# Kernel tuning notes

Measured on AMD Instinct MI355X. Metric: run time of the kernel, lower is better.

Reference implementation:

```python
import jax, jax.numpy as jnp
import numpy as np

EMBED_DIM = 128
NUM_HEADS = 4
HEAD_DIM = EMBED_DIM // NUM_HEADS


def setup_inputs() -> dict:
    key = jax.random.key(0)
    ks = jax.random.split(key, 12)
    B, N, D = 4, 4096, EMBED_DIM
    s = 1.0 / np.sqrt(D)
    inp = {
        "query": jax.random.normal(ks[0], (B, N, D), dtype=jnp.float32),
        "key": jax.random.normal(ks[1], (B, N, D), dtype=jnp.float32),
        "value": jax.random.normal(ks[2], (B, N, D), dtype=jnp.float32),
        "Wq": jax.random.uniform(ks[3], (D, D), jnp.float32, -s, s),
        "bq": jax.random.uniform(ks[4], (D,), jnp.float32, -s, s),
        "Wk": jax.random.uniform(ks[5], (D, D), jnp.float32, -s, s),
        "bk": jax.random.uniform(ks[6], (D,), jnp.float32, -s, s),
        "Wv": jax.random.uniform(ks[7], (D, D), jnp.float32, -s, s),
        "bv": jax.random.uniform(ks[8], (D,), jnp.float32, -s, s),
        "Wo": jax.random.uniform(ks[9], (D, D), jnp.float32, -s, s),
        "bo": jax.random.uniform(ks[10], (D,), jnp.float32, -s, s),
    }
    return inp


def reference(query, key, value, Wq, bq, Wk, bk, Wv, bv, Wo, bo):
    B, N, D = query.shape
    H, Dh = NUM_HEADS, HEAD_DIM
    scale = Dh ** -0.5
    # Linear projections (torch Linear: x @ W.T + b), split heads -> [B, H, N, Dh]
    Q = (query @ Wq.T + bq).reshape(B, N, H, Dh).transpose(0, 2, 1, 3)
    K = (key @ Wk.T + bk).reshape(B, N, H, Dh).transpose(0, 2, 1, 3)
    V = (value @ Wv.T + bv).reshape(B, N, H, Dh).transpose(0, 2, 1, 3)
    # Attention scores [B, H, N, N]
    scores = jnp.einsum('bhqd,bhkd->bhqk', Q, K) * scale
    attn = jax.nn.softmax(scores, axis=-1)
    ctx = jnp.einsum('bhqk,bhkd->bhqd', attn, V)  # [B, H, N, Dh]
    ctx = ctx.transpose(0, 2, 1, 3).reshape(B, N, D)
    return ctx @ Wo.T + bo
```

## Files before the change

kernel.cpp:

```cpp
#include <hip/hip_runtime.h>
#include <hip/hip_bf16.h>

#define N_SEQ 4096
#define DIM   128
#define NH    4
#define DH    32
#define BATCH 4

#define QSCALE 0.25503495870989204f

typedef __bf16 bf16x8 __attribute__((ext_vector_type(8)));
typedef __bf16 bf16x2 __attribute__((ext_vector_type(2)));
typedef __bf16 bf16x4 __attribute__((ext_vector_type(4)));
typedef float  f32x4  __attribute__((ext_vector_type(4)));

#define MFMA(a, b, c) __builtin_amdgcn_mfma_f32_16x16x32_bf16((a), (b), (c), 0, 0, 0)

static __device__ __forceinline__ bf16x8 cvt8(const float* __restrict__ p) {
    const float4* f4 = reinterpret_cast<const float4*>(p);
    float4 a = f4[0], b = f4[1];
    bf16x8 r;
    r[0] = (__bf16)a.x; r[1] = (__bf16)a.y; r[2] = (__bf16)a.z; r[3] = (__bf16)a.w;
    r[4] = (__bf16)b.x; r[5] = (__bf16)b.y; r[6] = (__bf16)b.z; r[7] = (__bf16)b.w;
    return r;
}

static __device__ __forceinline__ f32x4 exp4(f32x4 s) {
    f32x4 r;
    r[0] = __builtin_amdgcn_exp2f(s[0]);
    r[1] = __builtin_amdgcn_exp2f(s[1]);
    r[2] = __builtin_amdgcn_exp2f(s[2]);
    r[3] = __builtin_amdgcn_exp2f(s[3]);
    return r;
}

static __device__ __forceinline__ bf16x8 pack8(f32x4 a, f32x4 b) {
    bf16x8 o;
    o[0] = (__bf16)a[0]; o[1] = (__bf16)a[1];
    o[2] = (__bf16)a[2]; o[3] = (__bf16)a[3];
    o[4] = (__bf16)b[0]; o[5] = (__bf16)b[1];
    o[6] = (__bf16)b[2]; o[7] = (__bf16)b[3];
    return o;
}

__global__ __launch_bounds__(256) void proj_qkv(
    const float* __restrict__ xq, const float* __restrict__ xk, const float* __restrict__ xv,
    const float* __restrict__ Wq, const float* __restrict__ Wk, const float* __restrict__ Wv,
    const float* __restrict__ bq, const float* __restrict__ bk, const float* __restrict__ bv,
    __bf16* __restrict__ Qs, __bf16* __restrict__ Kb, __bf16* __restrict__ Vt)
{
    __shared__ __align__(16) char wlds[34816];
    const int z = blockIdx.z;
    const float* x    = (z == 0) ? xq : ((z == 1) ? xk : xv);
    const float* Wf   = (z == 0) ? Wq : ((z == 1) ? Wk : Wv);
    const float* bias = (z == 0) ? bq : ((z == 1) ? bk : bv);
    const int b    = blockIdx.y;
    const int tid  = threadIdx.x;
    const int wave = tid >> 6, lane = tid & 63;
    const int quad = lane >> 4, l15 = lane & 15;
    const int n0   = blockIdx.x * 64 + wave * 16;

    {
        const int r = tid >> 1, half = tid & 1;
        const float* wsrc = Wf + r * DIM + half * 64;
        char* wdst = wlds + r * 272 + half * 128;
        #pragma unroll
        for (int i = 0; i < 8; i++)
            *(bf16x8*)(wdst + i * 16) = cvt8(wsrc + i * 8);
    }

    bf16x8 a[4];
    const float* xrow = x + (b * N_SEQ + n0 + l15) * DIM + quad * 8;
    a[0] = cvt8(xrow);      a[1] = cvt8(xrow + 32);
    a[2] = cvt8(xrow + 64); a[3] = cvt8(xrow + 96);
    __syncthreads();

    const int n = n0 + l15;
    for (int t = 0; t < 8; t++) {
        const char* wr = wlds + (t * 16 + l15) * 272 + quad * 16;
        bf16x8 w0 = *(const bf16x8*)(wr);
        bf16x8 w1 = *(const bf16x8*)(wr + 64);
        bf16x8 w2 = *(const bf16x8*)(wr + 128);
        bf16x8 w3 = *(const bf16x8*)(wr + 192);

        f32x4 acc = {0.f, 0.f, 0.f, 0.f};
        acc = MFMA(w0, a[0], acc);
        acc = MFMA(w1, a[1], acc);
        acc = MFMA(w2, a[2], acc);
        acc = MFMA(w3, a[3], acc);

        const int d0 = t * 16 + quad * 4;
        if (z == 0) {
            const int h = d0 >> 5, dh0 = d0 & 31;
            bf16x4 q4;
            #pragma unroll
            for (int r = 0; r < 4; r++)
                q4[r] = (__bf16)((acc[r] + bias[d0 + r]) * QSCALE);
            *(bf16x4*)(Qs + ((b * NH + h) * N_SEQ + n) * DH + dh0) = q4;
        } else if (z == 1) {
            const int h = d0 >> 5, dh0 = d0 & 31;
            bf16x4 k4;
            #pragma unroll
            for (int r = 0; r < 4; r++)
                k4[r] = (__bf16)(acc[r] + bias[d0 + r]);
            *(bf16x4*)(Kb + ((b * NH + h) * N_SEQ + n) * DH + dh0) = k4;
        } else {
            const int nl = n & 63;
            const int np = (n & ~63) | (nl & 35) | ((nl & 12) << 1) | ((nl & 16) >> 2);
            #pragma unroll
            for (int r = 0; r < 4; r++) {
                const int d = d0 + r, h = d >> 5, dh = d & 31;
                Vt[((b * NH + h) * DH + dh) * N_SEQ + np] = (__bf16)(acc[r] + bias[d]);
            }
        }
    }
}

__global__ __launch_bounds__(256, 2) void flash_attn(
    const __bf16* __restrict__ Qs, const __bf16* __restrict__ Kb,
    const __bf16* __restrict__ Vt, __bf16* __restrict__ ctxb)
{
    __shared__ __align__(16) char smem[77824];
    char* const Kbase = smem;
    char* const Vbase = smem + 40960;

    const int bid  = blockIdx.x;
    const int bh   = bid & 15;
    const int qc   = bid >> 4;
    const int tid  = threadIdx.x;
    const int wave = tid >> 6, lane = tid & 63;
    const int quad = lane >> 4, l15 = lane & 15;
    const int qh   = wave & 1, kh = wave >> 1;
    const int n0   = qc * 128 + qh * 64;
    const int KH   = 2048;

    const __bf16* Qp = Qs + (bh * N_SEQ + n0) * DH;
    bf16x8 qf[4];
    #pragma unroll
    for (int q = 0; q < 4; q++)
        qf[q] = *(const bf16x8*)(Qp + (q * 16 + l15) * DH + quad * 8);

    const int r_ = tid >> 2, c_ = tid & 3;
    const __bf16* gK = Kb + (size_t)bh * N_SEQ * DH + r_ * DH + c_ * 8;
    const __bf16* gV = Vt + ((size_t)bh * DH + (tid >> 3)) * N_SEQ + (tid & 7) * 8;
    const int kofsK = r_ * 80 + c_ * 16;
    const int kofsV = (tid >> 3) * 144 + (tid & 7) * 16;

    {
        #pragma unroll
        for (int g = 0; g < 2; g++) {
            #pragma unroll
            for (int t = 0; t < 2; t++) {
                bf16x8 kr = *(const bf16x8*)(gK + (size_t)(g * KH + t * 64) * DH);
                bf16x8 vr = *(const bf16x8*)(gV + g * KH + t * 64);
                *(bf16x8*)(Kbase + g * 20480 + t * 5120 + kofsK) = kr;
                *(bf16x8*)(Vbase + g * 18432 + t * 4608 + kofsV) = vr;
            }
        }
    }
    __syncthreads();

    char* const Kme = Kbase + kh * 20480;
    char* const Vme = Vbase + kh * 18432;

    f32x4 c[4][2];
    #pragma unroll
    for (int q = 0; q < 4; q++) { c[q][0] = f32x4{0.f,0.f,0.f,0.f}; c[q][1] = f32x4{0.f,0.f,0.f,0.f}; }
    float l[4] = {0.f, 0.f, 0.f, 0.f};
    const f32x4 z4 = {0.f,0.f,0.f,0.f};

    for (int kbb = 0; kbb < KH / 128; kbb++) {
        const int cur = kbb & 1;
        const char* Kc = Kme + cur * 10240;
        const char* Vc = Vme + cur * 9216;

        const int kn = (kbb + 1) & (KH / 128 - 1);
        bf16x8 krn[2][2], vrn[2][2];
        #pragma unroll
        for (int g = 0; g < 2; g++) {
            #pragma unroll
            for (int t = 0; t < 2; t++) {
                krn[g][t] = *(const bf16x8*)(gK + (size_t)(g * KH + kn * 128 + t * 64) * DH);
                vrn[g][t] = *(const bf16x8*)(gV + g * KH + kn * 128 + t * 64);
            }
        }

        #pragma unroll
        for (int t = 0; t < 2; t++) {
            const char* Kt  = Kc + t * 5120;
            const char* Vtl = Vc + t * 4608;

            bf16x8 kf0 = *(const bf16x8*)(Kt + l15 * 80 + quad * 16);
            bf16x8 kf1 = *(const bf16x8*)(Kt + (16 + l15) * 80 + quad * 16);
            bf16x8 kf2 = *(const bf16x8*)(Kt + (32 + l15) * 80 + quad * 16);
            bf16x8 kf3 = *(const bf16x8*)(Kt + (48 + l15) * 80 + quad * 16);

            bf16x8 pf[4][2];
            #pragma unroll
            for (int q = 0; q < 4; q++) {
                f32x4 sa = MFMA(kf0, qf[q], z4);
                f32x4 sb = MFMA(kf1, qf[q], z4);
                f32x4 sc = MFMA(kf2, qf[q], z4);
                f32x4 sd = MFMA(kf3, qf[q], z4);
                f32x4 ea = exp4(sa), eb = exp4(sb), ec = exp4(sc), ed = exp4(sd);
                l[q] += ((ea[0]+ea[1])+(ea[2]+ea[3])) + ((eb[0]+eb[1])+(eb[2]+eb[3]))
                      + ((ec[0]+ec[1])+(ec[2]+ec[3])) + ((ed[0]+ed[1])+(ed[2]+ed[3]));
                pf[q][0] = pack8(ea, eb);
                pf[q][1] = pack8(ec, ed);
            }

            bf16x8 vf00 = *(const bf16x8*)(Vtl + l15 * 144 + quad * 16);
            bf16x8 vf10 = *(const bf16x8*)(Vtl + (16 + l15) * 144 + quad * 16);
            bf16x8 vf01 = *(const bf16x8*)(Vtl + l15 * 144 + 64 + quad * 16);
            bf16x8 vf11 = *(const bf16x8*)(Vtl + (16 + l15) * 144 + 64 + quad * 16);

            #pragma unroll
            for (int q = 0; q < 4; q++) {
                c[q][0] = MFMA(vf00, pf[q][0], c[q][0]);
                c[q][1] = MFMA(vf10, pf[q][0], c[q][1]);
                c[q][0] = MFMA(vf01, pf[q][1], c[q][0]);
                c[q][1] = MFMA(vf11, pf[q][1], c[q][1]);
            }
        }

        #pragma unroll
        for (int g = 0; g < 2; g++) {
            #pragma unroll
            for (int t = 0; t < 2; t++) {
                *(bf16x8*)(Kbase + g * 20480 + (cur ^ 1) * 10240 + t * 5120 + kofsK) = krn[g][t];
                *(bf16x8*)(Vbase + g * 18432 + (cur ^ 1) * 9216 + t * 4608 + kofsV) = vrn[g][t];
            }
        }
        __syncthreads();
    }

    #pragma unroll
    for (int q = 0; q < 4; q++) {
        l[q] += __shfl_xor(l[q], 16);
        l[q] += __shfl_xor(l[q], 32);
    }

    if (kh == 1) {
        char* dst = smem + (qh * 64 + lane) * 144;
        #pragma unroll
        for (int q = 0; q < 4; q++) {
            *(f32x4*)(dst + (q * 2 + 0) * 16) = c[q][0];
            *(f32x4*)(dst + (q * 2 + 1) * 16) = c[q][1];
        }
        f32x4 lv = {l[0], l[1], l[2], l[3]};
        *(f32x4*)(dst + 128) = lv;
    }
    __syncthreads();
    if (kh == 0) {
        const char* src = smem + (qh * 64 + lane) * 144;
        f32x4 lp = *(const f32x4*)(src + 128);
        const int b = bh >> 2, h = bh & 3;
        #pragma unroll
        for (int q = 0; q < 4; q++) {
            c[q][0] += *(const f32x4*)(src + (q * 2 + 0) * 16);
            c[q][1] += *(const f32x4*)(src + (q * 2 + 1) * 16);
            const float inv = 1.0f / (l[q] + lp[q]);
            const int qg = n0 + q * 16 + l15;
            __bf16* dst = ctxb + ((size_t)(b * N_SEQ + qg)) * DIM + h * DH + quad * 4;
            #pragma unroll
            for (int dt = 0; dt < 2; dt++) {
                f32x4 cc = c[q][dt];
                bf16x2 e0 = {(__bf16)(cc[0] * inv), (__bf16)(cc[1] * inv)};
                bf16x2 e1 = {(__bf16)(cc[2] * inv), (__bf16)(cc[3] * inv)};
                *(bf16x2*)(dst + dt * 16)     = e0;
                *(bf16x2*)(dst + dt * 16 + 2) = e1;
            }
        }
    }
}

__global__ __launch_bounds__(256) void out_proj(
    const __bf16* __restrict__ ctxb, const float* __restrict__ Wo,
    const float* __restrict__ bo, float* __restrict__ out)
{
    __shared__ __align__(16) char wlds[34816];
    const int b    = blockIdx.y;
    const int tid  = threadIdx.x;
    const int wave = tid >> 6, lane = tid & 63;
    const int quad = lane >> 4, l15 = lane & 15;
    const int n0   = blockIdx.x * 64 + wave * 16;

    {
        const int r = tid >> 1, half = tid & 1;
        const float* wsrc = Wo + r * DIM + half * 64;
        char* wdst = wlds + r * 272 + half * 128;
        #pragma unroll
        for (int i = 0; i < 8; i++)
            *(bf16x8*)(wdst + i * 16) = cvt8(wsrc + i * 8);
    }

    bf16x8 a[4];
    const __bf16* crow = ctxb + (b * N_SEQ + n0 + l15) * DIM + quad * 8;
    a[0] = *(const bf16x8*)(crow);
    a[1] = *(const bf16x8*)(crow + 32);
    a[2] = *(const bf16x8*)(crow + 64);
    a[3] = *(const bf16x8*)(crow + 96);
    __syncthreads();

    const int n = n0 + l15;
    for (int t = 0; t < 8; t++) {
        const char* wr = wlds + (t * 16 + l15) * 272 + quad * 16;
        bf16x8 w0 = *(const bf16x8*)(wr);
        bf16x8 w1 = *(const bf16x8*)(wr + 64);
        bf16x8 w2 = *(const bf16x8*)(wr + 128);
        bf16x8 w3 = *(const bf16x8*)(wr + 192);

        f32x4 acc = {0.f, 0.f, 0.f, 0.f};
        acc = MFMA(w0, a[0], acc);
        acc = MFMA(w1, a[1], acc);
        acc = MFMA(w2, a[2], acc);
        acc = MFMA(w3, a[3], acc);

        const int d0 = t * 16 + quad * 4;
        float4 o;
        o.x = acc[0] + bo[d0];
        o.y = acc[1] + bo[d0 + 1];
        o.z = acc[2] + bo[d0 + 2];
        o.w = acc[3] + bo[d0 + 3];
        *(float4*)(out + (b * N_SEQ + n) * DIM + d0) = o;
    }
}

extern "C" void kernel_launch(void* const* d_in, const int* in_sizes, int n_in,
                              void* d_out, int out_size, void* d_ws, size_t ws_size,
                              hipStream_t stream)
{
    const float* query = (const float*)d_in[0];
    const float* key   = (const float*)d_in[1];
    const float* value = (const float*)d_in[2];
    const float* Wq = (const float*)d_in[3];
    const float* bq = (const float*)d_in[4];
    const float* Wk = (const float*)d_in[5];
    const float* bk = (const float*)d_in[6];
    const float* Wv = (const float*)d_in[7];
    const float* bv = (const float*)d_in[8];
    const float* Wo = (const float*)d_in[9];
    const float* bo = (const float*)d_in[10];
    float* out = (float*)d_out;

    char* ws = (char*)d_ws;
    const size_t e = (size_t)BATCH * N_SEQ * DIM;
    __bf16* Qs   = (__bf16*)(ws);
    __bf16* Kb   = (__bf16*)(ws + 2 * e);
    __bf16* Vt   = (__bf16*)(ws + 4 * e);
    __bf16* ctxb = (__bf16*)(ws + 6 * e);

    proj_qkv<<<dim3(64, BATCH, 3), 256, 0, stream>>>(
        query, key, value, Wq, Wk, Wv, bq, bk, bv, Qs, Kb, Vt);
    flash_attn<<<dim3(512), 256, 0, stream>>>(Qs, Kb, Vt, ctxb);
    out_proj<<<dim3(64, BATCH), 256, 0, stream>>>(ctxb, Wo, bo, out);
}
```

Measured before the change: 150.2 us.

## Split flash attention work across eight waves per block with 32-row query slices

Doubles the attention block to 512 threads so each wave handles 32 query rows instead of 64, halving per-wave accumulators and Q fragments. Loading is also split so the first 256 threads stage K tiles and the rest stage V tiles, giving one prefetch stream per thread. This is meant to raise waves per CU and hide MFMA/exp latency. The cost is that each K/V tile read from LDS is reused by fewer query rows, so LDS traffic per unit of work goes up, and the 76 KB of LDS per block limits how many blocks fit on a CU.

```diff
diff --git a/kernel.cpp b/kernel.cpp
--- a/kernel.cpp
+++ b/kernel.cpp
@@ -116,7 +116,7 @@
     }
 }
 
-__global__ __launch_bounds__(256, 2) void flash_attn(
+__global__ __launch_bounds__(512, 4) void flash_attn(
     const __bf16* __restrict__ Qs, const __bf16* __restrict__ Kb,
     const __bf16* __restrict__ Vt, __bf16* __restrict__ ctxb)
 {
@@ -130,31 +130,38 @@
     const int tid  = threadIdx.x;
     const int wave = tid >> 6, lane = tid & 63;
     const int quad = lane >> 4, l15 = lane & 15;
-    const int qh   = wave & 1, kh = wave >> 1;
-    const int n0   = qc * 128 + qh * 64;
+    const int qh   = wave & 3, kh = wave >> 2;
+    const int n0   = qc * 128 + qh * 32;
     const int KH   = 2048;
 
     const __bf16* Qp = Qs + (bh * N_SEQ + n0) * DH;
-    bf16x8 qf[4];
-    #pragma unroll
-    for (int q = 0; q < 4; q++)
-        qf[q] = *(const bf16x8*)(Qp + (q * 16 + l15) * DH + quad * 8);
-
-    const int r_ = tid >> 2, c_ = tid & 3;
-    const __bf16* gK = Kb + (size_t)bh * N_SEQ * DH + r_ * DH + c_ * 8;
-    const __bf16* gV = Vt + ((size_t)bh * DH + (tid >> 3)) * N_SEQ + (tid & 7) * 8;
-    const int kofsK = r_ * 80 + c_ * 16;
-    const int kofsV = (tid >> 3) * 144 + (tid & 7) * 16;
+    bf16x8 qf[2];
+    qf[0] = *(const bf16x8*)(Qp + l15 * DH + quad * 8);
+    qf[1] = *(const bf16x8*)(Qp + (16 + l15) * DH + quad * 8);
+
+    const int s = tid & 255;
+    const bool isK = (tid < 256);
+    const __bf16* gsrc;
+    char* ldsb;
+    int kofs, gstr, bstr, tstr;
+    size_t gmul;
+    if (isK) {
+        gsrc = Kb + (size_t)bh * N_SEQ * DH + (s >> 2) * DH + (s & 3) * 8;
+        ldsb = Kbase; kofs = (s >> 2) * 80 + (s & 3) * 16;
+        gstr = 20480; bstr = 10240; tstr = 5120; gmul = DH;
+    } else {
+        gsrc = Vt + ((size_t)bh * DH + (s >> 3)) * N_SEQ + (s & 7) * 8;
+        ldsb = Vbase; kofs = (s >> 3) * 144 + (s & 7) * 16;
+        gstr = 18432; bstr = 9216; tstr = 4608; gmul = 1;
+    }
 
     {
         #pragma unroll
         for (int g = 0; g < 2; g++) {
             #pragma unroll
             for (int t = 0; t < 2; t++) {
-                bf16x8 kr = *(const bf16x8*)(gK + (size_t)(g * KH + t * 64) * DH);
-                bf16x8 vr = *(const bf16x8*)(gV + g * KH + t * 64);
-                *(bf16x8*)(Kbase + g * 20480 + t * 5120 + kofsK) = kr;
-                *(bf16x8*)(Vbase + g * 18432 + t * 4608 + kofsV) = vr;
+                bf16x8 r = *(const bf16x8*)(gsrc + (size_t)(g * KH + t * 64) * gmul);
+                *(bf16x8*)(ldsb + g * gstr + t * tstr + kofs) = r;
             }
         }
     }
@@ -163,11 +170,10 @@
     char* const Kme = Kbase + kh * 20480;
     char* const Vme = Vbase + kh * 18432;
 
-    f32x4 c[4][2];
-    #pragma unroll
-    for (int q = 0; q < 4; q++) { c[q][0] = f32x4{0.f,0.f,0.f,0.f}; c[q][1] = f32x4{0.f,0.f,0.f,0.f}; }
-    float l[4] = {0.f, 0.f, 0.f, 0.f};
-    const f32x4 z4 = {0.f,0.f,0.f,0.f};
+    f32x4 c[2][2];
+    const f32x4 z4 = {0.f, 0.f, 0.f, 0.f};
+    c[0][0] = z4; c[0][1] = z4; c[1][0] = z4; c[1][1] = z4;
+    float l[2] = {0.f, 0.f};
 
     for (int kbb = 0; kbb < KH / 128; kbb++) {
         const int cur = kbb & 1;
@@ -175,14 +181,12 @@
         const char* Vc = Vme + cur * 9216;
 
         const int kn = (kbb + 1) & (KH / 128 - 1);
-        bf16x8 krn[2][2], vrn[2][2];
+        bf16x8 pre[2][2];
         #pragma unroll
         for (int g = 0; g < 2; g++) {
             #pragma unroll
-            for (int t = 0; t < 2; t++) {
-                krn[g][t] = *(const bf16x8*)(gK + (size_t)(g * KH + kn * 128 + t * 64) * DH);
-                vrn[g][t] = *(const bf16x8*)(gV + g * KH + kn * 128 + t * 64);
-            }
+            for (int t = 0; t < 2; t++)
+                pre[g][t] = *(const bf16x8*)(gsrc + (size_t)(g * KH + kn * 128 + t * 64) * gmul);
         }
 
         #pragma unroll
@@ -195,9 +199,9 @@
             bf16x8 kf2 = *(const bf16x8*)(Kt + (32 + l15) * 80 + quad * 16);
             bf16x8 kf3 = *(const bf16x8*)(Kt + (48 + l15) * 80 + quad * 16);
 
-            bf16x8 pf[4][2];
-            #pragma unroll
-            for (int q = 0; q < 4; q++) {
+            bf16x8 pf[2][2];
+            #pragma unroll
+            for (int q = 0; q < 2; q++) {
                 f32x4 sa = MFMA(kf0, qf[q], z4);
                 f32x4 sb = MFMA(kf1, qf[q], z4);
                 f32x4 sc = MFMA(kf2, qf[q], z4);
@@ -215,7 +219,7 @@
             bf16x8 vf11 = *(const bf16x8*)(Vtl + (16 + l15) * 144 + 64 + quad * 16);
 
             #pragma unroll
-            for (int q = 0; q < 4; q++) {
+            for (int q = 0; q < 2; q++) {
                 c[q][0] = MFMA(vf00, pf[q][0], c[q][0]);
                 c[q][1] = MFMA(vf10, pf[q][0], c[q][1]);
                 c[q][0] = MFMA(vf01, pf[q][1], c[q][0]);
@@ -226,40 +230,39 @@
         #pragma unroll
         for (int g = 0; g < 2; g++) {
             #pragma unroll
-            for (int t = 0; t < 2; t++) {
-                *(bf16x8*)(Kbase + g * 20480 + (cur ^ 1) * 10240 + t * 5120 + kofsK) = krn[g][t];
-                *(bf16x8*)(Vbase + g * 18432 + (cur ^ 1) * 9216 + t * 4608 + kofsV) = vrn[g][t];
-            }
+            for (int t = 0; t < 2; t++)
+                *(bf16x8*)(ldsb + g * gstr + (cur ^ 1) * bstr + t * tstr + kofs) = pre[g][t];
         }
         __syncthreads();
     }
 
     #pragma unroll
-    for (int q = 0; q < 4; q++) {
+    for (int q = 0; q < 2; q++) {
         l[q] += __shfl_xor(l[q], 16);
         l[q] += __shfl_xor(l[q], 32);
     }
 
     if (kh == 1) {
-        char* dst = smem + (qh * 64 + lane) * 144;
-        #pragma unroll
-        for (int q = 0; q < 4; q++) {
-            *(f32x4*)(dst + (q * 2 + 0) * 16) = c[q][0];
-            *(f32x4*)(dst + (q * 2 + 1) * 16) = c[q][1];
-        }
-        f32x4 lv = {l[0], l[1], l[2], l[3]};
-        *(f32x4*)(dst + 128) = lv;
+        char* dst = smem + (qh * 64 + lane) * 80;
+        #pragma unroll
+        for (int q = 0; q < 2; q++) {
+            *(f32x4*)(dst + q * 32)      = c[q][0];
+            *(f32x4*)(dst + q * 32 + 16) = c[q][1];
+        }
+        float2 lv = {l[0], l[1]};
+        *(float2*)(dst + 64) = lv;
     }
     __syncthreads();
     if (kh == 0) {
-        const char* src = smem + (qh * 64 + lane) * 144;
-        f32x4 lp = *(const f32x4*)(src + 128);
+        const char* src = smem + (qh * 64 + lane) * 80;
+        float2 lp = *(const float2*)(src + 64);
+        const float lpa[2] = {lp.x, lp.y};
         const int b = bh >> 2, h = bh & 3;
         #pragma unroll
-        for (int q = 0; q < 4; q++) {
-            c[q][0] += *(const f32x4*)(src + (q * 2 + 0) * 16);
-            c[q][1] += *(const f32x4*)(src + (q * 2 + 1) * 16);
-            const float inv = 1.0f / (l[q] + lp[q]);
+        for (int q = 0; q < 2; q++) {
+            c[q][0] += *(const f32x4*)(src + q * 32);
+            c[q][1] += *(const f32x4*)(src + q * 32 + 16);
+            const float inv = 1.0f / (l[q] + lpa[q]);
             const int qg = n0 + q * 16 + l15;
             __bf16* dst = ctxb + ((size_t)(b * N_SEQ + qg)) * DIM + h * DH + quad * 4;
             #pragma unroll
@@ -352,6 +355,6 @@
 
     proj_qkv<<<dim3(64, BATCH, 3), 256, 0, stream>>>(
         query, key, value, Wq, Wk, Wv, bq, bk, bv, Qs, Kb, Vt);
-    flash_attn<<<dim3(512), 256, 0, stream>>>(Qs, Kb, Vt, ctxb);
+    flash_attn<<<dim3(512), 512, 0, stream>>>(Qs, Kb, Vt, ctxb);
     out_proj<<<dim3(64, BATCH), 256, 0, stream>>>(ctxb, Wo, bo, out);
 }
```

New measurement: 158.2 us. +5.3%, slower.

## Compute softmax row sums with ones-matrix MFMA and prioritize MFMA issue

Applied to the files above, without the earlier changes.

Moves the softmax denominator accumulation off the VALU by multiplying the packed bf16 probabilities with a ones vector through extra MFMAs. This drops the per-element adds and the final cross-lane shuffles. All K/V LDS fragments for both sub-tiles are now loaded before compute, and MFMA sections are wrapped in s_setprio to favour matrix issue. The change adds 25% more PV-stage MFMAs, raises register pressure from the preloaded fragments, and sums the bf16-rounded probabilities rather than the fp32 ones.

```diff
diff --git a/kernel.cpp b/kernel.cpp
--- a/kernel.cpp
+++ b/kernel.cpp
@@ -140,6 +140,10 @@
     for (int q = 0; q < 4; q++)
         qf[q] = *(const bf16x8*)(Qp + (q * 16 + l15) * DH + quad * 8);
 
+    bf16x8 ones;
+    #pragma unroll
+    for (int i = 0; i < 8; i++) ones[i] = (__bf16)1.0f;
+
     const int r_ = tid >> 2, c_ = tid & 3;
     const __bf16* gK = Kb + (size_t)bh * N_SEQ * DH + r_ * DH + c_ * 8;
     const __bf16* gV = Vt + ((size_t)bh * DH + (tid >> 3)) * N_SEQ + (tid & 7) * 8;
@@ -164,10 +168,10 @@
     char* const Vme = Vbase + kh * 18432;
 
     f32x4 c[4][2];
+    f32x4 cl[4];
+    const f32x4 z4 = {0.f,0.f,0.f,0.f};
     #pragma unroll
-    for (int q = 0; q < 4; q++) { c[q][0] = f32x4{0.f,0.f,0.f,0.f}; c[q][1] = f32x4{0.f,0.f,0.f,0.f}; }
-    float l[4] = {0.f, 0.f, 0.f, 0.f};
-    const f32x4 z4 = {0.f,0.f,0.f,0.f};
+    for (int q = 0; q < 4; q++) { c[q][0] = z4; c[q][1] = z4; cl[q] = z4; }
 
     for (int kbb = 0; kbb < KH / 128; kbb++) {
         const int cur = kbb & 1;
@@ -185,42 +189,47 @@
             }
         }
 
+        bf16x8 kfa[2][4], vfa[2][4];
         #pragma unroll
         for (int t = 0; t < 2; t++) {
             const char* Kt  = Kc + t * 5120;
             const char* Vtl = Vc + t * 4608;
-
-            bf16x8 kf0 = *(const bf16x8*)(Kt + l15 * 80 + quad * 16);
-            bf16x8 kf1 = *(const bf16x8*)(Kt + (16 + l15) * 80 + quad * 16);
-            bf16x8 kf2 = *(const bf16x8*)(Kt + (32 + l15) * 80 + quad * 16);
-            bf16x8 kf3 = *(const bf16x8*)(Kt + (48 + l15) * 80 + quad * 16);
-
+            #pragma unroll
+            for (int i = 0; i < 4; i++)
+                kfa[t][i] = *(const bf16x8*)(Kt + (i * 16 + l15) * 80 + quad * 16);
+            vfa[t][0] = *(const bf16x8*)(Vtl + l15 * 144 + quad * 16);
+            vfa[t][1] = *(const bf16x8*)(Vtl + (16 + l15) * 144 + quad * 16);
+            vfa[t][2] = *(const bf16x8*)(Vtl + l15 * 144 + 64 + quad * 16);
+            vfa[t][3] = *(const bf16x8*)(Vtl + (16 + l15) * 144 + 64 + quad * 16);
+        }
+
+        #pragma unroll
+        for (int t = 0; t < 2; t++) {
             bf16x8 pf[4][2];
             #pragma unroll
             for (int q = 0; q < 4; q++) {
-                f32x4 sa = MFMA(kf0, qf[q], z4);
-                f32x4 sb = MFMA(kf1, qf[q], z4);
-                f32x4 sc = MFMA(kf2, qf[q], z4);
-                f32x4 sd = MFMA(kf3, qf[q], z4);
+                __builtin_amdgcn_s_setprio(1);
+                f32x4 sa = MFMA(kfa[t][0], qf[q], z4);
+                f32x4 sb = MFMA(kfa[t][1], qf[q], z4);
+                f32x4 sc = MFMA(kfa[t][2], qf[q], z4);
+                f32x4 sd = MFMA(kfa[t][3], qf[q], z4);
+                __builtin_amdgcn_s_setprio(0);
                 f32x4 ea = exp4(sa), eb = exp4(sb), ec = exp4(sc), ed = exp4(sd);
-                l[q] += ((ea[0]+ea[1])+(ea[2]+ea[3])) + ((eb[0]+eb[1])+(eb[2]+eb[3]))
-                      + ((ec[0]+ec[1])+(ec[2]+ec[3])) + ((ed[0]+ed[1])+(ed[2]+ed[3]));
                 pf[q][0] = pack8(ea, eb);
                 pf[q][1] = pack8(ec, ed);
             }
 
-            bf16x8 vf00 = *(const bf16x8*)(Vtl + l15 * 144 + quad * 16);
-            bf16x8 vf10 = *(const bf16x8*)(Vtl + (16 + l15) * 144 + quad * 16);
-            bf16x8 vf01 = *(const bf16x8*)(Vtl + l15 * 144 + 64 + quad * 16);
-            bf16x8 vf11 = *(const bf16x8*)(Vtl + (16 + l15) * 144 + 64 + quad * 16);
-
+            __builtin_amdgcn_s_setprio(1);
             #pragma unroll
             for (int q = 0; q < 4; q++) {
-                c[q][0] = MFMA(vf00, pf[q][0], c[q][0]);
-                c[q][1] = MFMA(vf10, pf[q][0], c[q][1]);
-                c[q][0] = MFMA(vf01, pf[q][1], c[q][0]);
-                c[q][1] = MFMA(vf11, pf[q][1], c[q][1]);
-            }
+                c[q][0] = MFMA(vfa[t][0], pf[q][0], c[q][0]);
+                c[q][1] = MFMA(vfa[t][1], pf[q][0], c[q][1]);
+                c[q][0] = MFMA(vfa[t][2], pf[q][1], c[q][0]);
+                c[q][1] = MFMA(vfa[t][3], pf[q][1], c[q][1]);
+                cl[q]   = MFMA(ones, pf[q][0], cl[q]);
+                cl[q]   = MFMA(ones, pf[q][1], cl[q]);
+            }
+            __builtin_amdgcn_s_setprio(0);
         }
 
         #pragma unroll
@@ -234,11 +243,6 @@
         __syncthreads();
     }
 
-    #pragma unroll
-    for (int q = 0; q < 4; q++) {
-        l[q] += __shfl_xor(l[q], 16);
-        l[q] += __shfl_xor(l[q], 32);
-    }
 
     if (kh == 1) {
         char* dst = smem + (qh * 64 + lane) * 144;
@@ -247,7 +251,7 @@
             *(f32x4*)(dst + (q * 2 + 0) * 16) = c[q][0];
             *(f32x4*)(dst + (q * 2 + 1) * 16) = c[q][1];
         }
-        f32x4 lv = {l[0], l[1], l[2], l[3]};
+        f32x4 lv = {cl[0][0], cl[1][0], cl[2][0], cl[3][0]};
         *(f32x4*)(dst + 128) = lv;
     }
     __syncthreads();
@@ -259,7 +263,7 @@
         for (int q = 0; q < 4; q++) {
             c[q][0] += *(const f32x4*)(src + (q * 2 + 0) * 16);
             c[q][1] += *(const f32x4*)(src + (q * 2 + 1) * 16);
-            const float inv = 1.0f / (l[q] + lp[q]);
+            const float inv = 1.0f / (cl[q][0] + lp[q]);
             const int qg = n0 + q * 16 + l15;
             __bf16* dst = ctxb + ((size_t)(b * N_SEQ + qg)) * DIM + h * DH + quad * 4;
             #pragma unroll
```

New measurement: 147.4 us. Within noise of the previous version (-1.9%).
